# Kernel optimization log

Hardware: AMD Instinct MI355X
Metric: run time of the kernel (lower is better)

Reference implementation:

```python
import jax, jax.numpy as jnp
import numpy as np

N_NODES = 100000
N_EDGES = 3200000
PERIODS = 12
C_IN, C_OUT, F_OUT = 1, 4, 12


def setup_inputs() -> dict:
    key = jax.random.key(0)
    ks = jax.random.split(key, 20)
    s = 0.1
    return {
        "x": jax.random.normal(ks[0], (N_NODES, C_IN, PERIODS), dtype=jnp.float32),
        "edge_index": jax.random.randint(ks[1], (2, N_EDGES), 0, N_NODES, dtype=jnp.int32),
        "conv_z_w": s * jax.random.normal(ks[2], (C_IN, C_OUT), dtype=jnp.float32),
        "conv_z_b": s * jax.random.normal(ks[3], (C_OUT,), dtype=jnp.float32),
        "lin_z_w": s * jax.random.normal(ks[4], (2 * C_OUT, C_OUT), dtype=jnp.float32),
        "lin_z_b": s * jax.random.normal(ks[5], (C_OUT,), dtype=jnp.float32),
        "conv_r_w": s * jax.random.normal(ks[6], (C_IN, C_OUT), dtype=jnp.float32),
        "conv_r_b": s * jax.random.normal(ks[7], (C_OUT,), dtype=jnp.float32),
        "lin_r_w": s * jax.random.normal(ks[8], (2 * C_OUT, C_OUT), dtype=jnp.float32),
        "lin_r_b": s * jax.random.normal(ks[9], (C_OUT,), dtype=jnp.float32),
        "conv_h_w": s * jax.random.normal(ks[10], (C_IN, C_OUT), dtype=jnp.float32),
        "conv_h_b": s * jax.random.normal(ks[11], (C_OUT,), dtype=jnp.float32),
        "lin_h_w": s * jax.random.normal(ks[12], (2 * C_OUT, C_OUT), dtype=jnp.float32),
        "lin_h_b": s * jax.random.normal(ks[13], (C_OUT,), dtype=jnp.float32),
        "att": jax.random.normal(ks[14], (PERIODS,), dtype=jnp.float32),
        "out_w": s * jax.random.normal(ks[15], (C_OUT, F_OUT), dtype=jnp.float32),
        "out_b": s * jax.random.normal(ks[16], (F_OUT,), dtype=jnp.float32),
        "f": 12,
    }


def reference(x, edge_index, conv_z_w, conv_z_b, lin_z_w, lin_z_b,
              conv_r_w, conv_r_b, lin_r_w, lin_r_b,
              conv_h_w, conv_h_b, lin_h_w, lin_h_b,
              att, out_w, out_b, f):
    N, _, P = x.shape
    loops = jnp.arange(N, dtype=edge_index.dtype)
    src = jnp.concatenate([edge_index[0], loops])  # self loops, fill=1
    dst = jnp.concatenate([edge_index[1], loops])
    deg = jax.ops.segment_sum(jnp.ones_like(src, dtype=x.dtype), dst, num_segments=N)
    dinv = jnp.where(deg > 0, jax.lax.rsqrt(deg), 0.0)
    norm = dinv[src] * dinv[dst]  # [E+N] symmetric GCN normalization

    def gcn(xt, W, b):
        xw = xt @ W  # [N, C_OUT]
        msg = xw[src] * norm[:, None]
        return jax.ops.segment_sum(msg, dst, num_segments=N) + b

    H0 = jnp.zeros((N, conv_z_w.shape[1]), dtype=x.dtype)

    def tgcn_step(xt):  # xt: [N, C_IN]; A3TGCN does not carry H across periods
        z = jax.nn.sigmoid(jnp.concatenate([gcn(xt, conv_z_w, conv_z_b), H0], 1) @ lin_z_w + lin_z_b)
        r = jax.nn.sigmoid(jnp.concatenate([gcn(xt, conv_r_w, conv_r_b), H0], 1) @ lin_r_w + lin_r_b)
        h_t = jnp.tanh(jnp.concatenate([gcn(xt, conv_h_w, conv_h_b), r * H0], 1) @ lin_h_w + lin_h_b)
        return z * H0 + (1.0 - z) * h_t

    xs = jnp.transpose(x, (2, 0, 1))  # [P, N, C_IN]
    Hs = jax.vmap(tgcn_step)(xs)  # [P, N, C_OUT]
    probs = jax.nn.softmax(att)
    H_accum = jnp.einsum('p,pnd->nd', probs, Hs)  # attention over periods
    out = H_accum @ out_w + out_b  # [N, 12]
    return out[:, :f]
```

## Files before the change

### kernel.cpp

```cpp
#include <hip/hip_runtime.h>
#include <hip/hip_fp16.h>
#include <math.h>


#define PERIODS 12
#define BSZ     256
#define BSH     8
#define STRIDE  13312
#define SLICE   3328
#define NSLICE  4
#define SRCBITS 17
#define SMASK   ((1 << SRCBITS) - 1)
#define CH      8192
#define NT      1024
#define ACCW    7
#define BIAS_F  262144.f

struct Consts {
    float az[4], cz[4], ah[4], ch[4], probs[PERIODS];
};

typedef float vf2 __attribute__((ext_vector_type(2)));

__device__ __forceinline__ float dec1_manual(unsigned b) {
    unsigned e = (b >> 3) & 15u, m = b & 7u;
    float v = e ? __uint_as_float(((e + 120u) << 23) | (m << 20))
                : (float)m * 0.001953125f;
    return (b & 0x80u) ? -v : v;
}

__device__ __forceinline__ void dec4(unsigned u, float* o) {
#if __has_builtin(__builtin_amdgcn_cvt_pk_f32_fp8)
    vf2 lo = __builtin_amdgcn_cvt_pk_f32_fp8((int)u, false);
    vf2 hi = __builtin_amdgcn_cvt_pk_f32_fp8((int)u, true);
    o[0] = lo.x; o[1] = lo.y; o[2] = hi.x; o[3] = hi.y;
#else
    o[0] = dec1_manual(u & 255u);
    o[1] = dec1_manual((u >> 8) & 255u);
    o[2] = dec1_manual((u >> 16) & 255u);
    o[3] = dec1_manual(u >> 24);
#endif
}

__device__ __forceinline__ unsigned enc1_manual(float x) {
    unsigned s = (__float_as_uint(x) >> 24) & 0x80u;
    float a = fabsf(x);
    if (!(a > 0.f)) return s;
    a = fminf(a, 448.f);
    int eb = (int)(__float_as_uint(a) >> 23) - 127;
    int e = eb < -6 ? -6 : eb;
    float q = rintf(a * exp2f((float)(3 - e)));
    if (q >= 16.f) { e++; q = rintf(a * exp2f((float)(3 - e))); }
    if (e > 8) return s | 0x7Eu;
    int m = (int)q;
    unsigned ee, mm;
    if (m >= 8) { ee = (unsigned)(e + 7); mm = (unsigned)(m - 8); }
    else        { ee = 0u; mm = (unsigned)m; }
    return s | (ee << 3) | mm;
}

__device__ __forceinline__ unsigned pk4(float a, float b, float c, float d) {
#if __has_builtin(__builtin_amdgcn_cvt_pk_fp8_f32)
    int v = __builtin_amdgcn_cvt_pk_fp8_f32(a, b, 0, false);
    v = __builtin_amdgcn_cvt_pk_fp8_f32(c, d, v, true);
    return (unsigned)v;
#else
    return enc1_manual(a) | (enc1_manual(b) << 8) |
           (enc1_manual(c) << 16) | (enc1_manual(d) << 24);
#endif
}


__global__ __launch_bounds__(512) void k_setup(const float* conv_z_w, const float* conv_z_b,
                        const float* lin_z_w, const float* lin_z_b,
                        const float* conv_h_w, const float* conv_h_b,
                        const float* lin_h_w, const float* lin_h_b,
                        const float* att, Consts* C, int* gcur, int NB)
{
    int t = threadIdx.x;
    for (int i = t; i < NB; i += 512) gcur[i] = 0;
    if (t == 0) {
        for (int c = 0; c < 4; ++c) {
            float az = 0.f, cz = 0.f, ah = 0.f, ch = 0.f;
            for (int k = 0; k < 4; ++k) {
                az += conv_z_w[k] * lin_z_w[k * 4 + c];
                cz += conv_z_b[k] * lin_z_w[k * 4 + c];
                ah += conv_h_w[k] * lin_h_w[k * 4 + c];
                ch += conv_h_b[k] * lin_h_w[k * 4 + c];
            }
            C->az[c] = az; C->cz[c] = cz + lin_z_b[c];
            C->ah[c] = ah; C->ch[c] = ch + lin_h_b[c];
        }
        float m = att[0];
        for (int p = 1; p < PERIODS; ++p) m = fmaxf(m, att[p]);
        float e[PERIODS]; float s = 0.f;
        for (int p = 0; p < PERIODS; ++p) { e[p] = expf(att[p] - m); s += e[p]; }
        for (int p = 0; p < PERIODS; ++p) C->probs[p] = e[p] / s;
    }
}

__global__ __launch_bounds__(NT, 4) void k_binA(const int* __restrict__ ei,
                                                int* __restrict__ gcur,
                                                int* __restrict__ binned, int E, int N) {
    __shared__ int hist[512];
    __shared__ int scn[512];
    __shared__ int gdel[512];
    __shared__ int sv[CH];
    __shared__ int sa[CH];
    int t = threadIdx.x;
    if (t < 512) hist[t] = 0;
    __syncthreads();
    int base = blockIdx.x * CH;
    int lim = min(E - base, CH);
    int rs[CH / NT], rd[CH / NT];
    #pragma unroll
    for (int k = 0; k < CH / NT; ++k) {
        int i = t + k * NT;
        if (i < lim) {
            rs[k] = ei[base + i];
            rd[k] = ei[E + base + i];
            atomicAdd(&hist[rd[k] >> BSH], 1);
        }
    }
    __syncthreads();
    int v = 0;
    if (t < 512) { v = hist[t]; scn[t] = v; }
    __syncthreads();
    for (int off = 1; off < 512; off <<= 1) {
        int tmp = 0;
        if (t < 512 && t >= off) tmp = scn[t - off];
        __syncthreads();
        if (t < 512) scn[t] += tmp;
        __syncthreads();
    }
    int gbase = 0, vp = 0;
    if (t < 512) {
        int excl = scn[t] - v;
        vp = (v + 15) & ~15;
        int g = (vp > 0) ? atomicAdd(&gcur[t], vp) : 0;
        gbase = t * STRIDE + g;
        gdel[t] = gbase - excl;
        hist[t] = excl;
    }
    __syncthreads();
    #pragma unroll
    for (int k = 0; k < CH / NT; ++k) {
        int i = t + k * NT;
        if (i < lim) {
            int s = rs[k];
            int d = rd[k];
            int b = d >> BSH;
            int pos = atomicAdd(&hist[b], 1);
            sv[pos] = ((d & (BSZ - 1)) << SRCBITS) | s;
            sa[pos] = gdel[b] + pos;
        }
    }
    __syncthreads();
    for (int j = t; j < lim; j += NT)
        binned[sa[j]] = sv[j];
    if (t < 512) {
        for (int j = v; j < vp; ++j)
            binned[gbase + j] = N;
    }
}

__global__ __launch_bounds__(NT, 4) void k_degprep(const int* __restrict__ binned,
                                                   const int* __restrict__ gcur,
                                                   const float* __restrict__ x,
                                                   int* __restrict__ deg,
                                                   float* __restrict__ dinv,
                                                   uint4* __restrict__ xs8, int N) {
    __shared__ int hist[BSZ];
    int b = blockIdx.x, t = threadIdx.x;
    if (t < BSZ) hist[t] = 0;
    __syncthreads();
    int cnt = gcur[b];
    const int* bb = binned + b * STRIDE;
    for (int i = t; i < cnt; i += NT) {
        int pv = bb[i];
        if ((pv & SMASK) < N) atomicAdd(&hist[pv >> SRCBITS], 1);
    }
    __syncthreads();
    if (b == 0 && t == 0) xs8[N] = make_uint4(0, 0, 0, 0);
    if (t >= BSZ) return;
    int n = (b << BSH) + t;
    if (n >= N) return;
    int dg = hist[t];
    deg[n] = dg;
    float di = rsqrtf((float)dg + 1.0f);
    dinv[n] = di;
    const float4* xv = (const float4*)(x + (size_t)n * PERIODS);
    float4 v0 = xv[0], v1 = xv[1], v2 = xv[2];
    uint4 r;
    r.x = pk4(v0.x * di, v0.y * di, v0.z * di, v0.w * di);
    r.y = pk4(v1.x * di, v1.y * di, v1.z * di, v1.w * di);
    r.z = pk4(v2.x * di, v2.y * di, v2.z * di, v2.w * di);
    r.w = 0;
    xs8[n] = r;
}

__device__ __forceinline__ void scat(unsigned long long* acc, int d, uint4 r) {
    float f[PERIODS];
    dec4(r.x, f + 0); dec4(r.y, f + 4); dec4(r.z, f + 8);
    int base = d * ACCW;
    #pragma unroll
    for (int k = 0; k < 6; ++k) {
        unsigned lo = (unsigned)__float2int_rn(fmaf(f[k],     512.f, BIAS_F));
        unsigned hi = (unsigned)__float2int_rn(fmaf(f[k + 6], 512.f, BIAS_F));
        atomicAdd(&acc[base + k], ((unsigned long long)hi << 32) | (unsigned long long)lo);
    }
}

__global__ __launch_bounds__(512) void k_aggp(const int* __restrict__ binned,
                                              const int* __restrict__ gcur,
                                              const uint4* __restrict__ xs8,
                                              unsigned long long* __restrict__ pacc,
                                              int N) {
    __shared__ unsigned long long acc[BSZ * ACCW];
    int b = blockIdx.x >> 2, s = blockIdx.x & 3;
    int t = threadIdx.x;
    for (int i = t; i < BSZ * ACCW; i += 512) acc[i] = 0ull;
    __syncthreads();
    int cnt = gcur[b];
    int end = min(cnt, (s + 1) * SLICE);
    const int* bb = binned + b * STRIDE;
    int i = s * SLICE + t;
    for (; i + 512 < end; i += 1024) {
        int p0 = bb[i];
        int p1 = bb[i + 512];
        int s0 = p0 & SMASK, s1 = p1 & SMASK;
        uint4 r0 = xs8[s0];
        uint4 r1 = xs8[s1];
        if (s0 < N) scat(acc, p0 >> SRCBITS, r0);
        if (s1 < N) scat(acc, p1 >> SRCBITS, r1);
    }
    for (; i < end; i += 512) {
        int pv = bb[i];
        int sv = pv & SMASK;
        uint4 r = xs8[sv];
        if (sv < N) scat(acc, pv >> SRCBITS, r);
    }
    __syncthreads();
    unsigned long long* pb = pacc + (size_t)(b * NSLICE + s) * (BSZ * 6);
    for (int j = t; j < BSZ * 6; j += 512) {
        int node = j / 6, k = j - node * 6;
        pb[j] = acc[node * ACCW + k];
    }
}

__global__ __launch_bounds__(256) void k_merge(const unsigned long long* __restrict__ pacc,
                                               const int* __restrict__ deg,
                                               const float* __restrict__ dinv,
                                               const uint4* __restrict__ xs8,
                                               const Consts* __restrict__ C,
                                               const float* __restrict__ out_w,
                                               const float* __restrict__ out_b,
                                               float* __restrict__ out, int N) {
    int b = blockIdx.x, t = threadIdx.x;
    int n = (b << BSH) + t;
    if (n >= N) return;

    unsigned long long sum[6] = {0ull, 0ull, 0ull, 0ull, 0ull, 0ull};
    const unsigned long long* pb = pacc + (size_t)b * NSLICE * (BSZ * 6) + t * 6;
    #pragma unroll
    for (int s = 0; s < NSLICE; ++s) {
        #pragma unroll
        for (int k = 0; k < 6; ++k) sum[k] += pb[s * (BSZ * 6) + k];
    }

    int corr = deg[n] << 18;
    float a[PERIODS];
    {
        float f[PERIODS];
        uint4 r = xs8[n];
        dec4(r.x, f + 0); dec4(r.y, f + 4); dec4(r.z, f + 8);
        #pragma unroll
        for (int k = 0; k < 6; ++k) {
            int lo = (int)(unsigned)(sum[k] & 0xFFFFFFFFull) - corr;
            int hi = (int)(unsigned)(sum[k] >> 32) - corr;
            a[k]     = (float)lo * 0.001953125f + f[k];
            a[k + 6] = (float)hi * 0.001953125f + f[k + 6];
        }
    }

    float di = dinv[n];
    float hacc[4] = {0.f, 0.f, 0.f, 0.f};
    #pragma unroll
    for (int p = 0; p < PERIODS; ++p) {
        float ap = di * a[p];
        float pr = C->probs[p];
        #pragma unroll
        for (int c = 0; c < 4; ++c) {
            float zz = 1.f / (1.f + __expf(-(ap * C->az[c] + C->cz[c])));
            float hh = tanhf(ap * C->ah[c] + C->ch[c]);
            hacc[c] += pr * (1.f - zz) * hh;
        }
    }
    float o[PERIODS];
    #pragma unroll
    for (int f = 0; f < PERIODS; ++f) {
        float v = out_b[f];
        #pragma unroll
        for (int c = 0; c < 4; ++c) v += hacc[c] * out_w[c * PERIODS + f];
        o[f] = v;
    }
    float4* ov = (float4*)(out + (size_t)n * PERIODS);
    ov[0] = make_float4(o[0], o[1], o[2],  o[3]);
    ov[1] = make_float4(o[4], o[5], o[6],  o[7]);
    ov[2] = make_float4(o[8], o[9], o[10], o[11]);
}

extern "C" void kernel_launch(void* const* d_in, const int* in_sizes, int n_in,
                              void* d_out, int out_size, void* d_ws, size_t ws_size,
                              hipStream_t stream) {
    const float* x        = (const float*)d_in[0];
    const int*   ei       = (const int*)d_in[1];
    const float* conv_z_w = (const float*)d_in[2];
    const float* conv_z_b = (const float*)d_in[3];
    const float* lin_z_w  = (const float*)d_in[4];
    const float* lin_z_b  = (const float*)d_in[5];
    const float* conv_h_w = (const float*)d_in[10];
    const float* conv_h_b = (const float*)d_in[11];
    const float* lin_h_w  = (const float*)d_in[12];
    const float* lin_h_b  = (const float*)d_in[13];
    const float* att      = (const float*)d_in[14];
    const float* out_w    = (const float*)d_in[15];
    const float* out_b    = (const float*)d_in[16];
    float* out = (float*)d_out;

    const int N  = in_sizes[0] / PERIODS;
    const int E  = in_sizes[1] / 2;
    const int NB = (N + BSZ - 1) / BSZ;
    const int gA = (E + CH - 1) / CH;

    char* ws = (char*)d_ws;
    size_t off = 0;
    Consts* consts = (Consts*)(ws + off);  off += (sizeof(Consts) + 255) & ~255ull;
    int*    gcur   = (int*)(ws + off);     off += ((size_t)NB * 4 + 255) & ~255ull;
    int*    deg    = (int*)(ws + off);     off += ((size_t)N * 4 + 255) & ~255ull;
    float*  dinv   = (float*)(ws + off);   off += ((size_t)N * 4 + 255) & ~255ull;
    uint4*  xs8    = (uint4*)(ws + off);   off += ((size_t)(N + 256) * 16 + 255) & ~255ull;
    int*    binned = (int*)(ws + off);     off += ((size_t)NB * STRIDE * 4 + 255) & ~255ull;
    unsigned long long* pacc = (unsigned long long*)(ws + off);
    off += ((size_t)NB * NSLICE * BSZ * 6 * 8 + 255) & ~255ull;
    (void)ws_size; (void)n_in; (void)out_size;

    k_setup<<<1, 512, 0, stream>>>(conv_z_w, conv_z_b, lin_z_w, lin_z_b,
                                   conv_h_w, conv_h_b, lin_h_w, lin_h_b, att,
                                   consts, gcur, NB);
    k_binA<<<gA, NT, 0, stream>>>(ei, gcur, binned, E, N);
    k_degprep<<<NB, NT, 0, stream>>>(binned, gcur, x, deg, dinv, xs8, N);
    k_aggp<<<NB * NSLICE, 512, 0, stream>>>(binned, gcur, xs8, pacc, N);
    k_merge<<<NB, 256, 0, stream>>>(pacc, deg, dinv, xs8, consts,
                                    out_w, out_b, out, N);
}
```

Measured before the change: 163.2 us.

## Store pre-quantized fixed-point features instead of fp8 and drop setup kernel

Replaces the fp8-packed scaled features (16 bytes per node) with pre-biased 32-bit fixed-point integers (48 bytes per node). The aggregation kernel then does the 64-bit shared atomics straight from the loaded words, with no per-edge fp8 decode or float-to-int conversion. It also halves the slices per bin (two instead of four), replaces the setup kernel with a memset, and recomputes the folded gate constants and softmax in every merge thread. The cost is three times more gather traffic per edge. The padding entry at xs[N] is no longer zeroed, so padded reads fetch uninitialised memory, although their results are guarded out.

New measurement: 182.1 us. +11.6%, slower.

```diff
diff --git a/kernel.cpp b/kernel.cpp
--- a/kernel.cpp
+++ b/kernel.cpp
@@ -7,97 +7,15 @@
 #define BSZ     256
 #define BSH     8
 #define STRIDE  13312
-#define SLICE   3328
-#define NSLICE  4
+#define NSLICE  2
+#define SLICE   6656
 #define SRCBITS 17
 #define SMASK   ((1 << SRCBITS) - 1)
 #define CH      8192
 #define NT      1024
 #define ACCW    7
-#define BIAS_F  262144.f
-
-struct Consts {
-    float az[4], cz[4], ah[4], ch[4], probs[PERIODS];
-};
-
-typedef float vf2 __attribute__((ext_vector_type(2)));
-
-__device__ __forceinline__ float dec1_manual(unsigned b) {
-    unsigned e = (b >> 3) & 15u, m = b & 7u;
-    float v = e ? __uint_as_float(((e + 120u) << 23) | (m << 20))
-                : (float)m * 0.001953125f;
-    return (b & 0x80u) ? -v : v;
-}
-
-__device__ __forceinline__ void dec4(unsigned u, float* o) {
-#if __has_builtin(__builtin_amdgcn_cvt_pk_f32_fp8)
-    vf2 lo = __builtin_amdgcn_cvt_pk_f32_fp8((int)u, false);
-    vf2 hi = __builtin_amdgcn_cvt_pk_f32_fp8((int)u, true);
-    o[0] = lo.x; o[1] = lo.y; o[2] = hi.x; o[3] = hi.y;
-#else
-    o[0] = dec1_manual(u & 255u);
-    o[1] = dec1_manual((u >> 8) & 255u);
-    o[2] = dec1_manual((u >> 16) & 255u);
-    o[3] = dec1_manual(u >> 24);
-#endif
-}
-
-__device__ __forceinline__ unsigned enc1_manual(float x) {
-    unsigned s = (__float_as_uint(x) >> 24) & 0x80u;
-    float a = fabsf(x);
-    if (!(a > 0.f)) return s;
-    a = fminf(a, 448.f);
-    int eb = (int)(__float_as_uint(a) >> 23) - 127;
-    int e = eb < -6 ? -6 : eb;
-    float q = rintf(a * exp2f((float)(3 - e)));
-    if (q >= 16.f) { e++; q = rintf(a * exp2f((float)(3 - e))); }
-    if (e > 8) return s | 0x7Eu;
-    int m = (int)q;
-    unsigned ee, mm;
-    if (m >= 8) { ee = (unsigned)(e + 7); mm = (unsigned)(m - 8); }
-    else        { ee = 0u; mm = (unsigned)m; }
-    return s | (ee << 3) | mm;
-}
-
-__device__ __forceinline__ unsigned pk4(float a, float b, float c, float d) {
-#if __has_builtin(__builtin_amdgcn_cvt_pk_fp8_f32)
-    int v = __builtin_amdgcn_cvt_pk_fp8_f32(a, b, 0, false);
-    v = __builtin_amdgcn_cvt_pk_fp8_f32(c, d, v, true);
-    return (unsigned)v;
-#else
-    return enc1_manual(a) | (enc1_manual(b) << 8) |
-           (enc1_manual(c) << 16) | (enc1_manual(d) << 24);
-#endif
-}
-
-
-__global__ __launch_bounds__(512) void k_setup(const float* conv_z_w, const float* conv_z_b,
-                        const float* lin_z_w, const float* lin_z_b,
-                        const float* conv_h_w, const float* conv_h_b,
-                        const float* lin_h_w, const float* lin_h_b,
-                        const float* att, Consts* C, int* gcur, int NB)
-{
-    int t = threadIdx.x;
-    for (int i = t; i < NB; i += 512) gcur[i] = 0;
-    if (t == 0) {
-        for (int c = 0; c < 4; ++c) {
-            float az = 0.f, cz = 0.f, ah = 0.f, ch = 0.f;
-            for (int k = 0; k < 4; ++k) {
-                az += conv_z_w[k] * lin_z_w[k * 4 + c];
-                cz += conv_z_b[k] * lin_z_w[k * 4 + c];
-                ah += conv_h_w[k] * lin_h_w[k * 4 + c];
-                ch += conv_h_b[k] * lin_h_w[k * 4 + c];
-            }
-            C->az[c] = az; C->cz[c] = cz + lin_z_b[c];
-            C->ah[c] = ah; C->ch[c] = ch + lin_h_b[c];
-        }
-        float m = att[0];
-        for (int p = 1; p < PERIODS; ++p) m = fmaxf(m, att[p]);
-        float e[PERIODS]; float s = 0.f;
-        for (int p = 0; p < PERIODS; ++p) { e[p] = expf(att[p] - m); s += e[p]; }
-        for (int p = 0; p < PERIODS; ++p) C->probs[p] = e[p] / s;
-    }
-}
+#define BIAS_I  262144
+
 
 __global__ __launch_bounds__(NT, 4) void k_binA(const int* __restrict__ ei,
                                                 int* __restrict__ gcur,
@@ -169,7 +87,7 @@
                                                    const float* __restrict__ x,
                                                    int* __restrict__ deg,
                                                    float* __restrict__ dinv,
-                                                   uint4* __restrict__ xs8, int N) {
+                                                   uint4* __restrict__ xs48, int N) {
     __shared__ int hist[BSZ];
     int b = blockIdx.x, t = threadIdx.x;
     if (t < BSZ) hist[t] = 0;
@@ -181,7 +99,6 @@
         if ((pv & SMASK) < N) atomicAdd(&hist[pv >> SRCBITS], 1);
     }
     __syncthreads();
-    if (b == 0 && t == 0) xs8[N] = make_uint4(0, 0, 0, 0);
     if (t >= BSZ) return;
     int n = (b << BSH) + t;
     if (n >= N) return;
@@ -191,33 +108,25 @@
     dinv[n] = di;
     const float4* xv = (const float4*)(x + (size_t)n * PERIODS);
     float4 v0 = xv[0], v1 = xv[1], v2 = xv[2];
-    uint4 r;
-    r.x = pk4(v0.x * di, v0.y * di, v0.z * di, v0.w * di);
-    r.y = pk4(v1.x * di, v1.y * di, v1.z * di, v1.w * di);
-    r.z = pk4(v2.x * di, v2.y * di, v2.z * di, v2.w * di);
-    r.w = 0;
-    xs8[n] = r;
-}
-
-__device__ __forceinline__ void scat(unsigned long long* acc, int d, uint4 r) {
-    float f[PERIODS];
-    dec4(r.x, f + 0); dec4(r.y, f + 4); dec4(r.z, f + 8);
-    int base = d * ACCW;
-    #pragma unroll
-    for (int k = 0; k < 6; ++k) {
-        unsigned lo = (unsigned)__float2int_rn(fmaf(f[k],     512.f, BIAS_F));
-        unsigned hi = (unsigned)__float2int_rn(fmaf(f[k + 6], 512.f, BIAS_F));
-        atomicAdd(&acc[base + k], ((unsigned long long)hi << 32) | (unsigned long long)lo);
-    }
+    float f[PERIODS] = {v0.x, v0.y, v0.z, v0.w, v1.x, v1.y, v1.z, v1.w,
+                        v2.x, v2.y, v2.z, v2.w};
+    unsigned u[PERIODS];
+    #pragma unroll
+    for (int k = 0; k < PERIODS; ++k)
+        u[k] = (unsigned)(__float2int_rn(f[k] * di * 512.f) + BIAS_I);
+    uint4* row = xs48 + (size_t)n * 3;
+    row[0] = make_uint4(u[0], u[6], u[1], u[7]);
+    row[1] = make_uint4(u[2], u[8], u[3], u[9]);
+    row[2] = make_uint4(u[4], u[10], u[5], u[11]);
 }
 
 __global__ __launch_bounds__(512) void k_aggp(const int* __restrict__ binned,
                                               const int* __restrict__ gcur,
-                                              const uint4* __restrict__ xs8,
+                                              const uint4* __restrict__ xs48,
                                               unsigned long long* __restrict__ pacc,
                                               int N) {
     __shared__ unsigned long long acc[BSZ * ACCW];
-    int b = blockIdx.x >> 2, s = blockIdx.x & 3;
+    int b = blockIdx.x >> 1, s = blockIdx.x & 1;
     int t = threadIdx.x;
     for (int i = t; i < BSZ * ACCW; i += 512) acc[i] = 0ull;
     __syncthreads();
@@ -229,16 +138,43 @@
         int p0 = bb[i];
         int p1 = bb[i + 512];
         int s0 = p0 & SMASK, s1 = p1 & SMASK;
-        uint4 r0 = xs8[s0];
-        uint4 r1 = xs8[s1];
-        if (s0 < N) scat(acc, p0 >> SRCBITS, r0);
-        if (s1 < N) scat(acc, p1 >> SRCBITS, r1);
+        const uint4* r0 = xs48 + (size_t)s0 * 3;
+        const uint4* r1 = xs48 + (size_t)s1 * 3;
+        uint4 a0 = r0[0], a1 = r0[1], a2 = r0[2];
+        uint4 b0 = r1[0], b1 = r1[1], b2 = r1[2];
+        if (s0 < N) {
+            int ba = (p0 >> SRCBITS) * ACCW;
+            atomicAdd(&acc[ba + 0], ((unsigned long long)a0.y << 32) | a0.x);
+            atomicAdd(&acc[ba + 1], ((unsigned long long)a0.w << 32) | a0.z);
+            atomicAdd(&acc[ba + 2], ((unsigned long long)a1.y << 32) | a1.x);
+            atomicAdd(&acc[ba + 3], ((unsigned long long)a1.w << 32) | a1.z);
+            atomicAdd(&acc[ba + 4], ((unsigned long long)a2.y << 32) | a2.x);
+            atomicAdd(&acc[ba + 5], ((unsigned long long)a2.w << 32) | a2.z);
+        }
+        if (s1 < N) {
+            int ba = (p1 >> SRCBITS) * ACCW;
+            atomicAdd(&acc[ba + 0], ((unsigned long long)b0.y << 32) | b0.x);
+            atomicAdd(&acc[ba + 1], ((unsigned long long)b0.w << 32) | b0.z);
+            atomicAdd(&acc[ba + 2], ((unsigned long long)b1.y << 32) | b1.x);
+            atomicAdd(&acc[ba + 3], ((unsigned long long)b1.w << 32) | b1.z);
+            atomicAdd(&acc[ba + 4], ((unsigned long long)b2.y << 32) | b2.x);
+            atomicAdd(&acc[ba + 5], ((unsigned long long)b2.w << 32) | b2.z);
+        }
     }
     for (; i < end; i += 512) {
         int pv = bb[i];
         int sv = pv & SMASK;
-        uint4 r = xs8[sv];
-        if (sv < N) scat(acc, pv >> SRCBITS, r);
+        const uint4* r0 = xs48 + (size_t)sv * 3;
+        uint4 a0 = r0[0], a1 = r0[1], a2 = r0[2];
+        if (sv < N) {
+            int ba = (pv >> SRCBITS) * ACCW;
+            atomicAdd(&acc[ba + 0], ((unsigned long long)a0.y << 32) | a0.x);
+            atomicAdd(&acc[ba + 1], ((unsigned long long)a0.w << 32) | a0.z);
+            atomicAdd(&acc[ba + 2], ((unsigned long long)a1.y << 32) | a1.x);
+            atomicAdd(&acc[ba + 3], ((unsigned long long)a1.w << 32) | a1.z);
+            atomicAdd(&acc[ba + 4], ((unsigned long long)a2.y << 32) | a2.x);
+            atomicAdd(&acc[ba + 5], ((unsigned long long)a2.w << 32) | a2.z);
+        }
     }
     __syncthreads();
     unsigned long long* pb = pacc + (size_t)(b * NSLICE + s) * (BSZ * 6);
@@ -251,8 +187,16 @@
 __global__ __launch_bounds__(256) void k_merge(const unsigned long long* __restrict__ pacc,
                                                const int* __restrict__ deg,
                                                const float* __restrict__ dinv,
-                                               const uint4* __restrict__ xs8,
-                                               const Consts* __restrict__ C,
+                                               const uint4* __restrict__ xs48,
+                                               const float* __restrict__ conv_z_w,
+                                               const float* __restrict__ conv_z_b,
+                                               const float* __restrict__ lin_z_w,
+                                               const float* __restrict__ lin_z_b,
+                                               const float* __restrict__ conv_h_w,
+                                               const float* __restrict__ conv_h_b,
+                                               const float* __restrict__ lin_h_w,
+                                               const float* __restrict__ lin_h_b,
+                                               const float* __restrict__ att,
                                                const float* __restrict__ out_w,
                                                const float* __restrict__ out_b,
                                                float* __restrict__ out, int N) {
@@ -260,26 +204,54 @@
     int n = (b << BSH) + t;
     if (n >= N) return;
 
-    unsigned long long sum[6] = {0ull, 0ull, 0ull, 0ull, 0ull, 0ull};
-    const unsigned long long* pb = pacc + (size_t)b * NSLICE * (BSZ * 6) + t * 6;
-    #pragma unroll
-    for (int s = 0; s < NSLICE; ++s) {
-        #pragma unroll
-        for (int k = 0; k < 6; ++k) sum[k] += pb[s * (BSZ * 6) + k];
+    float az[4], cz[4], ah[4], ch[4];
+    #pragma unroll
+    for (int c = 0; c < 4; ++c) {
+        float a1 = 0.f, c1 = 0.f, a2 = 0.f, c2 = 0.f;
+        #pragma unroll
+        for (int k = 0; k < 4; ++k) {
+            a1 += conv_z_w[k] * lin_z_w[k * 4 + c];
+            c1 += conv_z_b[k] * lin_z_w[k * 4 + c];
+            a2 += conv_h_w[k] * lin_h_w[k * 4 + c];
+            c2 += conv_h_b[k] * lin_h_w[k * 4 + c];
+        }
+        az[c] = a1; cz[c] = c1 + lin_z_b[c];
+        ah[c] = a2; ch[c] = c2 + lin_h_b[c];
+    }
+    float probs[PERIODS];
+    {
+        float m = att[0];
+        #pragma unroll
+        for (int p = 1; p < PERIODS; ++p) m = fmaxf(m, att[p]);
+        float ssum = 0.f;
+        #pragma unroll
+        for (int p = 0; p < PERIODS; ++p) { probs[p] = expf(att[p] - m); ssum += probs[p]; }
+        float inv = 1.f / ssum;
+        #pragma unroll
+        for (int p = 0; p < PERIODS; ++p) probs[p] *= inv;
+    }
+
+    unsigned long long sum[6];
+    {
+        const unsigned long long* pb = pacc + (size_t)b * NSLICE * (BSZ * 6) + t * 6;
+        #pragma unroll
+        for (int k = 0; k < 6; ++k) sum[k] = pb[k] + pb[BSZ * 6 + k];
     }
 
     int corr = deg[n] << 18;
     float a[PERIODS];
     {
-        float f[PERIODS];
-        uint4 r = xs8[n];
-        dec4(r.x, f + 0); dec4(r.y, f + 4); dec4(r.z, f + 8);
+        const uint4* row = xs48 + (size_t)n * 3;
+        uint4 q0 = row[0], q1 = row[1], q2 = row[2];
+        int su[PERIODS] = {(int)q0.x, (int)q0.z, (int)q1.x, (int)q1.z,
+                           (int)q2.x, (int)q2.z, (int)q0.y, (int)q0.w,
+                           (int)q1.y, (int)q1.w, (int)q2.y, (int)q2.w};
         #pragma unroll
         for (int k = 0; k < 6; ++k) {
             int lo = (int)(unsigned)(sum[k] & 0xFFFFFFFFull) - corr;
             int hi = (int)(unsigned)(sum[k] >> 32) - corr;
-            a[k]     = (float)lo * 0.001953125f + f[k];
-            a[k + 6] = (float)hi * 0.001953125f + f[k + 6];
+            a[k]     = (float)(lo + su[k]     - BIAS_I) * 0.001953125f;
+            a[k + 6] = (float)(hi + su[k + 6] - BIAS_I) * 0.001953125f;
         }
     }
 
@@ -288,11 +260,11 @@
     #pragma unroll
     for (int p = 0; p < PERIODS; ++p) {
         float ap = di * a[p];
-        float pr = C->probs[p];
+        float pr = probs[p];
         #pragma unroll
         for (int c = 0; c < 4; ++c) {
-            float zz = 1.f / (1.f + __expf(-(ap * C->az[c] + C->cz[c])));
-            float hh = tanhf(ap * C->ah[c] + C->ch[c]);
+            float zz = 1.f / (1.f + __expf(-(ap * az[c] + cz[c])));
+            float hh = tanhf(ap * ah[c] + ch[c]);
             hacc[c] += pr * (1.f - zz) * hh;
         }
     }
@@ -335,22 +307,21 @@
 
     char* ws = (char*)d_ws;
     size_t off = 0;
-    Consts* consts = (Consts*)(ws + off);  off += (sizeof(Consts) + 255) & ~255ull;
     int*    gcur   = (int*)(ws + off);     off += ((size_t)NB * 4 + 255) & ~255ull;
     int*    deg    = (int*)(ws + off);     off += ((size_t)N * 4 + 255) & ~255ull;
     float*  dinv   = (float*)(ws + off);   off += ((size_t)N * 4 + 255) & ~255ull;
-    uint4*  xs8    = (uint4*)(ws + off);   off += ((size_t)(N + 256) * 16 + 255) & ~255ull;
+    uint4*  xs48   = (uint4*)(ws + off);   off += ((size_t)(N + 256) * 48 + 255) & ~255ull;
     int*    binned = (int*)(ws + off);     off += ((size_t)NB * STRIDE * 4 + 255) & ~255ull;
     unsigned long long* pacc = (unsigned long long*)(ws + off);
     off += ((size_t)NB * NSLICE * BSZ * 6 * 8 + 255) & ~255ull;
     (void)ws_size; (void)n_in; (void)out_size;
 
-    k_setup<<<1, 512, 0, stream>>>(conv_z_w, conv_z_b, lin_z_w, lin_z_b,
-                                   conv_h_w, conv_h_b, lin_h_w, lin_h_b, att,
-                                   consts, gcur, NB);
+    hipMemsetAsync(gcur, 0, (size_t)NB * 4, stream);
     k_binA<<<gA, NT, 0, stream>>>(ei, gcur, binned, E, N);
-    k_degprep<<<NB, NT, 0, stream>>>(binned, gcur, x, deg, dinv, xs8, N);
-    k_aggp<<<NB * NSLICE, 512, 0, stream>>>(binned, gcur, xs8, pacc, N);
-    k_merge<<<NB, 256, 0, stream>>>(pacc, deg, dinv, xs8, consts,
-                                    out_w, out_b, out, N);
-}
+    k_degprep<<<NB, NT, 0, stream>>>(binned, gcur, x, deg, dinv, xs48, N);
+    k_aggp<<<NB * NSLICE, 512, 0, stream>>>(binned, gcur, xs48, pacc, N);
+    k_merge<<<NB, 256, 0, stream>>>(pacc, deg, dinv, xs48,
+                                    conv_z_w, conv_z_b, lin_z_w, lin_z_b,
+                                    conv_h_w, conv_h_b, lin_h_w, lin_h_b,
+                                    att, out_w, out_b, out, N);
+}
```
